# Performance work log

Measured on AMD Instinct MI355X. Metric: run time of the kernel, lower is better.

Reference implementation:

```python
import jax, jax.numpy as jnp
import numpy as np

B, T, C = 16, 2048, 64  # n_embd = 64


def setup_inputs() -> dict:
    key = jax.random.key(0)
    ks = jax.random.split(key, 4)
    scale = 1.0 / np.sqrt(C)
    x = jax.random.normal(ks[0], (B, T, C), dtype=jnp.float32)
    Wk = jax.random.normal(ks[1], (C, C), dtype=jnp.float32) * scale
    Wq = jax.random.normal(ks[2], (C, C), dtype=jnp.float32) * scale
    Wv = jax.random.normal(ks[3], (C, C), dtype=jnp.float32) * scale
    bk = jnp.zeros((C,), dtype=jnp.float32)
    bq = jnp.zeros((C,), dtype=jnp.float32)
    bv = jnp.zeros((C,), dtype=jnp.float32)
    return {"x": x, "Wk": Wk, "bk": bk, "Wq": Wq, "bq": bq, "Wv": Wv, "bv": bv}


def reference(x, Wk, bk, Wq, bq, Wv, bv):
    # Faithful to source: wei = q @ k^T * C**0.5 (MULTIPLY, as in original code),
    # softmax over last axis, no causal mask (tril is built but unused), dropout=0.
    _, _, c = x.shape
    k = jnp.einsum('btc,cd->btd', x, Wk) + bk
    q = jnp.einsum('btc,cd->btd', x, Wq) + bq
    v = jnp.einsum('btc,cd->btd', x, Wv) + bv
    wei = jnp.einsum('btd,bsd->bts', q, k) * (c ** 0.5)  # [B,T,T]
    wei = jax.nn.softmax(wei, axis=-1)
    out = jnp.einsum('bts,bsd->btd', wei, v)  # [B,T,C]
    return out
```

## Files before the change

kernel.cpp:

```cpp
#include <hip/hip_runtime.h>
#include <hip/hip_bf16.h>
#include <stdint.h>

#define NBATCH 16
#define NT 2048
#define NC 64
#define QT 128
#define KT 128
#define SC_LOG2E 11.5415603f

typedef __bf16 bf16x8 __attribute__((ext_vector_type(8)));
typedef float f32x4 __attribute__((ext_vector_type(4)));
typedef float f32x16 __attribute__((ext_vector_type(16)));

#define Z16 {0.f,0.f,0.f,0.f,0.f,0.f,0.f,0.f,0.f,0.f,0.f,0.f,0.f,0.f,0.f,0.f}

extern "C" __device__ float __ocml_native_exp2_f32(float);
#define EXP2F(x) __ocml_native_exp2_f32(x)

static __device__ __forceinline__ unsigned short f2bf(float f) {
  __bf16 h = (__bf16)f;
  union { __bf16 h; unsigned short u; } a; a.h = h; return a.u;
}
static __device__ __forceinline__ float bf2f(unsigned short h) {
  union { uint32_t u; float f; } a; a.u = ((uint32_t)h) << 16;
  return a.f;
}
static __device__ __forceinline__ float fasu(uint32_t u) {
  union { uint32_t u; float f; } a; a.u = u; return a.f;
}
static __device__ __forceinline__ uint32_t uasf(float f) {
  union { float f; uint32_t u; } a; a.f = f; return a.u;
}

#define GLD_LDS16(gsrc, ldst)                                                  \
  __builtin_amdgcn_global_load_lds(                                            \
      (const __attribute__((address_space(1))) void*)(gsrc),                   \
      (__attribute__((address_space(3))) void*)(ldst), 16, 0, 0)

__global__ __launch_bounds__(256, 2) void prep_w(
    const float* __restrict__ Wk, const float* __restrict__ Wq,
    const float* __restrict__ Wv,
    unsigned short* __restrict__ wt_hi, unsigned short* __restrict__ wt_lo)
{
  __shared__ unsigned short hbuf[64][66];
  __shared__ unsigned short lbuf[64][66];
  const int m = (int)blockIdx.x;
  const float* Wm = (m == 0) ? Wk : (m == 1 ? Wq : Wv);
  const int tid = (int)threadIdx.x;
  for (int idx = tid; idx < 1024; idx += 256) {
    int c = idx >> 4, o4 = (idx & 15) * 4;
    float4 v = *(const float4*)(Wm + c * 64 + o4);
    float vals[4] = {v.x, v.y, v.z, v.w};
#pragma unroll
    for (int j = 0; j < 4; ++j) {
      unsigned short h = f2bf(vals[j]);
      hbuf[o4 + j][c] = h;
      lbuf[o4 + j][c] = f2bf(vals[j] - bf2f(h));
    }
  }
  __syncthreads();
  for (int idx = tid; idx < 1024; idx += 256) {
    int o = idx >> 4, c0 = (idx & 15) * 4;
    ushort4 hv, lv;
    hv.x = hbuf[o][c0]; hv.y = hbuf[o][c0 + 1];
    hv.z = hbuf[o][c0 + 2]; hv.w = hbuf[o][c0 + 3];
    lv.x = lbuf[o][c0]; lv.y = lbuf[o][c0 + 1];
    lv.z = lbuf[o][c0 + 2]; lv.w = lbuf[o][c0 + 3];
    *(ushort4*)(wt_hi + (size_t)(m * 64 + o) * 64 + c0) = hv;
    *(ushort4*)(wt_lo + (size_t)(m * 64 + o) * 64 + c0) = lv;
  }
}

__global__ __launch_bounds__(256, 2) void proj_kernel(
    const float* __restrict__ x,
    const unsigned short* __restrict__ wt_hi, const unsigned short* __restrict__ wt_lo,
    const float* __restrict__ bk, const float* __restrict__ bq, const float* __restrict__ bv,
    unsigned short* __restrict__ khi, unsigned short* __restrict__ klo,
    unsigned short* __restrict__ qhi, unsigned short* __restrict__ qlo,
    unsigned short* __restrict__ vt)
{
  __shared__ __align__(16) char smem[65536];
  const int XH = 0, XL = 8192, WTH = 16384, WTL = 40960, VTB = 0;
  const int tid = (int)threadIdx.x;
  const int l = tid & 63, w = tid >> 6;
  const int lr = l & 15, lg = l >> 4;
  const int blk = (int)blockIdx.x;
  const int rowbase = blk * 64;
  const int bb = blk >> 5;

  float4 xv[4];
#pragma unroll
  for (int j = 0; j < 4; ++j) {
    int c = tid + j * 256;
    int row = c >> 4, d0 = (c & 15) * 4;
    xv[j] = *(const float4*)(x + (size_t)(rowbase + row) * NC + d0);
  }
#pragma unroll
  for (int ch4 = 0; ch4 < 6; ++ch4) {
    int ch = ch4 * 4 + w;
    int d = ch * 1024 + l * 16;
    int swk = d ^ (((d >> 7) & 7) << 4);
    GLD_LDS16((const char*)wt_hi + swk, smem + WTH + ch * 1024);
    GLD_LDS16((const char*)wt_lo + swk, smem + WTL + ch * 1024);
  }
#pragma unroll
  for (int j = 0; j < 4; ++j) {
    int c = tid + j * 256;
    int row = c >> 4, d0 = (c & 15) * 4;
    unsigned short h0 = f2bf(xv[j].x), h1 = f2bf(xv[j].y), h2 = f2bf(xv[j].z), h3 = f2bf(xv[j].w);
    unsigned short m0 = f2bf(xv[j].x - bf2f(h0)), m1 = f2bf(xv[j].y - bf2f(h1));
    unsigned short m2 = f2bf(xv[j].z - bf2f(h2)), m3 = f2bf(xv[j].w - bf2f(h3));
    uint2 ph, pl;
    ph.x = (uint32_t)h0 | ((uint32_t)h1 << 16); ph.y = (uint32_t)h2 | ((uint32_t)h3 << 16);
    pl.x = (uint32_t)m0 | ((uint32_t)m1 << 16); pl.y = (uint32_t)m2 | ((uint32_t)m3 << 16);
    int byteoff = (row * 128 + d0 * 2) ^ ((row & 7) << 4);
    *(uint2*)(smem + XH + byteoff) = ph;
    *(uint2*)(smem + XL + byteoff) = pl;
  }
  __syncthreads();

  bf16x8 xh[2], xl[2];
  {
    int row = w * 16 + lr;
#pragma unroll
    for (int dc = 0; dc < 2; ++dc) {
      int byteoff = (row * 128 + (dc * 32 + lg * 8) * 2) ^ ((row & 7) << 4);
      xh[dc] = *(const bf16x8*)(smem + XH + byteoff);
      xl[dc] = *(const bf16x8*)(smem + XL + byteoff);
    }
  }
  f32x4 acc[12];
#pragma unroll
  for (int nb = 0; nb < 12; ++nb) {
    f32x4 a = {0.f, 0.f, 0.f, 0.f};
    int og = nb * 16 + lr;
#pragma unroll
    for (int dc = 0; dc < 2; ++dc) {
      int byteoff = (og * 128 + (dc * 32 + lg * 8) * 2) ^ ((og & 7) << 4);
      bf16x8 bh = *(const bf16x8*)(smem + WTH + byteoff);
      bf16x8 bl = *(const bf16x8*)(smem + WTL + byteoff);
      a = __builtin_amdgcn_mfma_f32_16x16x32_bf16(bh, xh[dc], a, 0, 0, 0);
      a = __builtin_amdgcn_mfma_f32_16x16x32_bf16(bl, xh[dc], a, 0, 0, 0);
      a = __builtin_amdgcn_mfma_f32_16x16x32_bf16(bh, xl[dc], a, 0, 0, 0);
    }
    acc[nb] = a;
  }
  __syncthreads();

  const int tloc = w * 16 + lr;
  const size_t gt = (size_t)(rowbase + tloc);
#pragma unroll
  for (int nb = 0; nb < 12; ++nb) {
    int ogb = (nb & 3) * 16 + lg * 4;
    const float* bp = (nb < 4) ? bk : (nb < 8 ? bq : bv);
    float4 bias = *(const float4*)(bp + ogb);
    float v0 = acc[nb][0] + bias.x, v1 = acc[nb][1] + bias.y,
          v2 = acc[nb][2] + bias.z, v3 = acc[nb][3] + bias.w;
    if (nb < 8) {
      if (nb >= 4) { v0 *= SC_LOG2E; v1 *= SC_LOG2E; v2 *= SC_LOG2E; v3 *= SC_LOG2E; }
      ushort4 hv, lv;
      hv.x = f2bf(v0); lv.x = f2bf(v0 - bf2f(hv.x));
      hv.y = f2bf(v1); lv.y = f2bf(v1 - bf2f(hv.y));
      hv.z = f2bf(v2); lv.z = f2bf(v2 - bf2f(hv.z));
      hv.w = f2bf(v3); lv.w = f2bf(v3 - bf2f(hv.w));
      unsigned short* dH = (nb < 4) ? khi : qhi;
      unsigned short* dL = (nb < 4) ? klo : qlo;
      *(ushort4*)(dH + gt * 64 + ogb) = hv;
      *(ushort4*)(dL + gt * 64 + ogb) = lv;
    } else {
      float vs[4] = {v0, v1, v2, v3};
#pragma unroll
      for (int r = 0; r < 4; ++r) {
        int o = ogb + r;
        int byteoff = (o * 128 + tloc * 2) ^ ((o & 7) << 4);
        *(unsigned short*)(smem + VTB + byteoff) = f2bf(vs[r]);
      }
    }
  }
  __syncthreads();
  for (int cc = tid; cc < 512; cc += 256) {
    int o = cc >> 3, t0 = (cc & 7) * 8;
    int byteoff = (o * 128 + t0 * 2) ^ ((o & 7) << 4);
    uint4 v = *(const uint4*)(smem + VTB + byteoff);
    *(uint4*)(vt + ((size_t)bb * 64 + o) * NT + (size_t)(blk & 31) * 64 + t0) = v;
  }
}

__global__ __launch_bounds__(1024, 4) void attn_kernel(
    const unsigned short* __restrict__ khi, const unsigned short* __restrict__ klo,
    const unsigned short* __restrict__ qhi, const unsigned short* __restrict__ qlo,
    const unsigned short* __restrict__ vt,
    float* __restrict__ out)
{
  __shared__ __align__(16) char smem[98304];
  const int BUF = 49152;
  const int MLB = 65536;
  const int tid = (int)threadIdx.x;
  const int l = tid & 63, w = tid >> 6;
  const int lq = l & 31;
  const bool hi = (l >= 32);
  const int hioff = hi ? 16 : 0;
  const int r = w & 3;
  const int cc = w >> 2;
  const int lb = ((int)(blockIdx.x & 7) << 5) | ((int)blockIdx.x >> 3);
  const int bb = lb >> 4;
  const int qt = lb & 15;

  const char* kh_base = (const char*)(khi + (size_t)bb * NT * 64);
  const char* kl_base = (const char*)(klo + (size_t)bb * NT * 64);
  const char* v_base  = (const char*)(vt + (size_t)bb * 64 * NT);

#define STAGE_TILE(bufp_, it_)                                                 \
  do {                                                                         \
    const char* kh_t = kh_base + (size_t)(it_) * 16384;                        \
    const char* kl_t = kl_base + (size_t)(it_) * 16384;                        \
    const char* v_tb = v_base + (size_t)(it_) * 256;                           \
    int d_ = w * 1024 + l * 16;                                                \
    int swk_ = d_ ^ (((d_ >> 7) & 7) << 4);                                    \
    GLD_LDS16(kh_t + swk_, (bufp_) + w * 1024);                                \
    GLD_LDS16(kl_t + swk_, (bufp_) + 16384 + w * 1024);                        \
    int o_ = d_ >> 8;                                                          \
    int swv_ = (d_ & 255) ^ ((o_ & 7) << 4);                                   \
    GLD_LDS16(v_tb + (size_t)o_ * 4096 + swv_, (bufp_) + 32768 + w * 1024);    \
  } while (0)

  STAGE_TILE(smem, 0);
  bf16x8 Qh[4], Ql[4];
  {
    const char* qh_t = (const char*)qhi + ((size_t)bb * NT + (size_t)qt * QT) * 128;
    const char* ql_t = (const char*)qlo + ((size_t)bb * NT + (size_t)qt * QT) * 128;
    int qrow = r * 32 + lq;
#pragma unroll
    for (int dc = 0; dc < 4; ++dc) {
      Qh[dc] = *(const bf16x8*)(qh_t + qrow * 128 + dc * 32 + hioff);
      Ql[dc] = *(const bf16x8*)(ql_t + qrow * 128 + dc * 32 + hioff);
    }
  }
  asm volatile("s_waitcnt vmcnt(0)" ::: "memory");
  __builtin_amdgcn_s_barrier();
  asm volatile("" ::: "memory");

  f32x16 O0 = Z16, O1 = Z16;
  float mrun = -1e30f, lrun = 0.f;
  const int swr = (lq & 7) << 4;

  for (int it = 0; it < NT / KT; ++it) {
    char* cb = smem + (it & 1) * BUF;
    if (it + 1 < NT / KT) STAGE_TILE(smem + ((it + 1) & 1) * BUF, it + 1);

    f32x16 S = Z16;
    __builtin_amdgcn_s_setprio(1);
#pragma unroll
    for (int dc = 0; dc < 4; ++dc) {
      int krow = cc * 32 + lq;
      int cchunk = (dc * 32 + hioff) ^ swr;
      bf16x8 Ah = *(const bf16x8*)(cb + krow * 128 + cchunk);
      bf16x8 Al = *(const bf16x8*)(cb + 16384 + krow * 128 + cchunk);
      S = __builtin_amdgcn_mfma_f32_32x32x16_bf16(Ah, Qh[dc], S, 0, 0, 0);
      S = __builtin_amdgcn_mfma_f32_32x32x16_bf16(Al, Qh[dc], S, 0, 0, 0);
      S = __builtin_amdgcn_mfma_f32_32x32x16_bf16(Ah, Ql[dc], S, 0, 0, 0);
    }
    __builtin_amdgcn_s_setprio(0);

    float m01 = fmaxf(S[0], S[1]),   m23 = fmaxf(S[2], S[3]);
    float m45 = fmaxf(S[4], S[5]),   m67 = fmaxf(S[6], S[7]);
    float m89 = fmaxf(S[8], S[9]),   mab = fmaxf(S[10], S[11]);
    float mcd = fmaxf(S[12], S[13]), mef = fmaxf(S[14], S[15]);
    float pmax = fmaxf(fmaxf(fmaxf(m01, m23), fmaxf(m45, m67)),
                       fmaxf(fmaxf(m89, mab), fmaxf(mcd, mef)));
    {
      auto sw = __builtin_amdgcn_permlane32_swap(uasf(pmax), uasf(pmax), false, false);
      pmax = fmaxf(fasu(sw[0]), fasu(sw[1]));
    }
    if (__any(pmax > mrun + 11.55f)) {
      float mnew = fmaxf(mrun, pmax);
      float alpha = EXP2F(mrun - mnew);
      O0 *= alpha; O1 *= alpha; lrun *= alpha; mrun = mnew;
    }
    float p[16];
#pragma unroll
    for (int i = 0; i < 16; ++i) p[i] = EXP2F(S[i] - mrun);
    float s01 = p[0] + p[1],   s23 = p[2] + p[3];
    float s45 = p[4] + p[5],   s67 = p[6] + p[7];
    float s89 = p[8] + p[9],   sab = p[10] + p[11];
    float scd = p[12] + p[13], sef = p[14] + p[15];
    float ts = ((s01 + s23) + (s45 + s67)) + ((s89 + sab) + (scd + sef));
    {
      auto sw = __builtin_amdgcn_permlane32_swap(uasf(ts), uasf(ts), false, false);
      ts = fasu(sw[0]) + fasu(sw[1]);
    }
    lrun += ts;

#define PV_CHUNK(kc_)                                                          \
    {                                                                          \
      const int b_ = 8 * (kc_);                                                \
      uint32_t X0, X1, Y0, Y1;                                                 \
      asm("v_cvt_pk_bf16_f32 %0, %1, %2" : "=v"(X0) : "v"(p[b_+0]), "v"(p[b_+1])); \
      asm("v_cvt_pk_bf16_f32 %0, %1, %2" : "=v"(X1) : "v"(p[b_+2]), "v"(p[b_+3])); \
      asm("v_cvt_pk_bf16_f32 %0, %1, %2" : "=v"(Y0) : "v"(p[b_+4]), "v"(p[b_+5])); \
      asm("v_cvt_pk_bf16_f32 %0, %1, %2" : "=v"(Y1) : "v"(p[b_+6]), "v"(p[b_+7])); \
      auto sw0 = __builtin_amdgcn_permlane32_swap(X0, Y0, false, false);       \
      auto sw1 = __builtin_amdgcn_permlane32_swap(X1, Y1, false, false);       \
      union { uint32_t u[4]; bf16x8 v; } cvb;                                  \
      cvb.u[0] = sw0[0]; cvb.u[1] = sw1[0];                                    \
      cvb.u[2] = sw0[1]; cvb.u[3] = sw1[1];                                    \
      bf16x8 Bp = cvb.v;                                                       \
      int vcol = 64 * cc + 32 * (kc_) + hioff;                                 \
      {                                                                        \
        bf16x8 Av = *(const bf16x8*)(cb + 32768 + lq * 256 + (vcol ^ swr));    \
        O0 = __builtin_amdgcn_mfma_f32_32x32x16_bf16(Av, Bp, O0, 0, 0, 0);     \
      }                                                                        \
      {                                                                        \
        bf16x8 Av = *(const bf16x8*)(cb + 32768 + (32 + lq) * 256 + (vcol ^ swr)); \
        O1 = __builtin_amdgcn_mfma_f32_32x32x16_bf16(Av, Bp, O1, 0, 0, 0);     \
      }                                                                        \
    }
    __builtin_amdgcn_s_setprio(1);
    PV_CHUNK(0)
    PV_CHUNK(1)
    __builtin_amdgcn_s_setprio(0);
#undef PV_CHUNK

    asm volatile("s_waitcnt vmcnt(0)" ::: "memory");
    __builtin_amdgcn_s_barrier();
    asm volatile("" ::: "memory");
    __builtin_amdgcn_sched_barrier(0);
  }

  const int lsw = (l & 7) << 4;
#define DUMP(idx_)                                                             \
  {                                                                            \
    char* dd = smem + (idx_) * 8192 + l * 128;                                 \
    _Pragma("unroll")                                                          \
    for (int g = 0; g < 4; ++g) {                                              \
      f32x4 t0, t1;                                                            \
      _Pragma("unroll")                                                        \
      for (int j = 0; j < 4; ++j) { t0[j] = O0[4*g+j]; t1[j] = O1[4*g+j]; }    \
      *(f32x4*)(dd + ((g * 16) ^ lsw)) = t0;                                   \
      *(f32x4*)(dd + ((64 + g * 16) ^ lsw)) = t1;                              \
    }                                                                          \
    *(float*)(smem + MLB + (idx_) * 256 + lq * 8) = mrun;                      \
    *(float*)(smem + MLB + (idx_) * 256 + lq * 8 + 4) = lrun;                  \
  }
#define MERGE(idx_)                                                            \
  {                                                                            \
    const char* ds = smem + (idx_) * 8192 + l * 128;                           \
    float m1 = *(const float*)(smem + MLB + (idx_) * 256 + lq * 8);            \
    float l1 = *(const float*)(smem + MLB + (idx_) * 256 + lq * 8 + 4);        \
    float M = fmaxf(mrun, m1);                                                 \
    float a0 = EXP2F(mrun - M);                                                \
    float a1 = EXP2F(m1 - M);                                                  \
    lrun = lrun * a0 + l1 * a1;                                                \
    mrun = M;                                                                  \
    _Pragma("unroll")                                                          \
    for (int g = 0; g < 4; ++g) {                                              \
      f32x4 o1a = *(const f32x4*)(ds + ((g * 16) ^ lsw));                      \
      f32x4 o1b = *(const f32x4*)(ds + ((64 + g * 16) ^ lsw));                 \
      _Pragma("unroll")                                                        \
      for (int j = 0; j < 4; ++j) {                                            \
        O0[4*g+j] = O0[4*g+j] * a0 + o1a[j] * a1;                              \
        O1[4*g+j] = O1[4*g+j] * a0 + o1b[j] * a1;                              \
      }                                                                        \
    }                                                                          \
  }
  if (cc & 1) DUMP(r * 2 + (cc >> 1));
  __syncthreads();
  if (!(cc & 1)) MERGE(r * 2 + (cc >> 1));
  __syncthreads();
  if (cc == 2) DUMP(r * 2 + 1);
  __syncthreads();
  if (cc == 0) {
    MERGE(r * 2 + 1);
    float inv = 1.0f / lrun;
    float* orow = out + ((size_t)bb * NT + (size_t)qt * QT + r * 32 + lq) * 64;
#pragma unroll
    for (int g = 0; g < 4; ++g) {
      int d0 = 8 * g + (hi ? 4 : 0);
      f32x4 s0, s1;
#pragma unroll
      for (int j = 0; j < 4; ++j) { s0[j] = O0[4*g+j] * inv; s1[j] = O1[4*g+j] * inv; }
      *(f32x4*)(orow + d0) = s0;
      *(f32x4*)(orow + d0 + 32) = s1;
    }
  }
#undef DUMP
#undef MERGE
#undef STAGE_TILE
}

extern "C" void kernel_launch(void* const* d_in, const int* in_sizes, int n_in,
                              void* d_out, int out_size, void* d_ws, size_t ws_size,
                              hipStream_t stream) {
  const float* x  = (const float*)d_in[0];
  const float* Wk = (const float*)d_in[1];
  const float* bk = (const float*)d_in[2];
  const float* Wq = (const float*)d_in[3];
  const float* bq = (const float*)d_in[4];
  const float* Wv = (const float*)d_in[5];
  const float* bv = (const float*)d_in[6];
  float* out = (float*)d_out;

  const size_t NE = (size_t)NBATCH * NT * 64;
  unsigned short* ws = (unsigned short*)d_ws;
  unsigned short* khi = ws;
  unsigned short* klo = ws + NE;
  unsigned short* qhi = ws + 2 * NE;
  unsigned short* qlo = ws + 3 * NE;
  unsigned short* vt  = ws + 4 * NE;
  unsigned short* wt_hi = ws + 5 * NE;
  unsigned short* wt_lo = wt_hi + 192 * 64;

  prep_w<<<dim3(3), dim3(256), 0, stream>>>(Wk, Wq, Wv, wt_hi, wt_lo);
  proj_kernel<<<dim3((NBATCH * NT) / 64), dim3(256), 0, stream>>>(
      x, wt_hi, wt_lo, bk, bq, bv, khi, klo, qhi, qlo, vt);
  attn_kernel<<<dim3(NBATCH * (NT / QT)), dim3(1024), 0, stream>>>(
      khi, klo, qhi, qlo, vt, out);
}
```

Baseline: 67.34 us.

## Switch attention operands to fp16 with single K and two-term Q split

Stores K, Q and V in fp16 rather than bf16. K becomes a single fp16 copy, dropping the K lo term, so QK^T needs two MFMAs per chunk instead of three, and the K staging traffic is halved. The query tile shrinks to 64 rows, with 512-thread blocks and a smaller LDS footprint, giving twice as many blocks. fp16 has less range than bf16, which could matter for the large scaled logits, and the smaller query tile means K/V tiles are reloaded more often per query.

```diff
diff --git a/kernel.cpp b/kernel.cpp
--- a/kernel.cpp
+++ b/kernel.cpp
@@ -5,11 +5,12 @@
 #define NBATCH 16
 #define NT 2048
 #define NC 64
-#define QT 128
+#define QT 64
 #define KT 128
 #define SC_LOG2E 11.5415603f
 
 typedef __bf16 bf16x8 __attribute__((ext_vector_type(8)));
+typedef _Float16 f16x8 __attribute__((ext_vector_type(8)));
 typedef float f32x4 __attribute__((ext_vector_type(4)));
 typedef float f32x16 __attribute__((ext_vector_type(16)));
 
@@ -26,11 +27,22 @@
   union { uint32_t u; float f; } a; a.u = ((uint32_t)h) << 16;
   return a.f;
 }
+static __device__ __forceinline__ unsigned short f2h(float f) {
+  _Float16 h = (_Float16)f;
+  union { _Float16 h; unsigned short u; } a; a.h = h; return a.u;
+}
+static __device__ __forceinline__ float h2f(unsigned short u) {
+  union { unsigned short u; _Float16 h; } a; a.u = u; return (float)a.h;
+}
 static __device__ __forceinline__ float fasu(uint32_t u) {
   union { uint32_t u; float f; } a; a.u = u; return a.f;
 }
 static __device__ __forceinline__ uint32_t uasf(float f) {
   union { float f; uint32_t u; } a; a.f = f; return a.u;
+}
+static __device__ __forceinline__ uint32_t pkh(float a, float b) {
+  auto h = __builtin_amdgcn_cvt_pkrtz(a, b);
+  union { decltype(h) v; uint32_t u; } c; c.v = h; return c.u;
 }
 
 #define GLD_LDS16(gsrc, ldst)                                                  \
@@ -76,9 +88,8 @@
     const float* __restrict__ x,
     const unsigned short* __restrict__ wt_hi, const unsigned short* __restrict__ wt_lo,
     const float* __restrict__ bk, const float* __restrict__ bq, const float* __restrict__ bv,
-    unsigned short* __restrict__ khi, unsigned short* __restrict__ klo,
-    unsigned short* __restrict__ qhi, unsigned short* __restrict__ qlo,
-    unsigned short* __restrict__ vt)
+    unsigned short* __restrict__ kf, unsigned short* __restrict__ qfh,
+    unsigned short* __restrict__ qfl, unsigned short* __restrict__ vt)
 {
   __shared__ __align__(16) char smem[65536];
   const int XH = 0, XL = 8192, WTH = 16384, WTL = 40960, VTB = 0;
@@ -157,24 +168,26 @@
     float4 bias = *(const float4*)(bp + ogb);
     float v0 = acc[nb][0] + bias.x, v1 = acc[nb][1] + bias.y,
           v2 = acc[nb][2] + bias.z, v3 = acc[nb][3] + bias.w;
-    if (nb < 8) {
-      if (nb >= 4) { v0 *= SC_LOG2E; v1 *= SC_LOG2E; v2 *= SC_LOG2E; v3 *= SC_LOG2E; }
+    if (nb < 4) {
+      ushort4 hv;
+      hv.x = f2h(v0); hv.y = f2h(v1); hv.z = f2h(v2); hv.w = f2h(v3);
+      *(ushort4*)(kf + gt * 64 + ogb) = hv;
+    } else if (nb < 8) {
+      v0 *= SC_LOG2E; v1 *= SC_LOG2E; v2 *= SC_LOG2E; v3 *= SC_LOG2E;
       ushort4 hv, lv;
-      hv.x = f2bf(v0); lv.x = f2bf(v0 - bf2f(hv.x));
-      hv.y = f2bf(v1); lv.y = f2bf(v1 - bf2f(hv.y));
-      hv.z = f2bf(v2); lv.z = f2bf(v2 - bf2f(hv.z));
-      hv.w = f2bf(v3); lv.w = f2bf(v3 - bf2f(hv.w));
-      unsigned short* dH = (nb < 4) ? khi : qhi;
-      unsigned short* dL = (nb < 4) ? klo : qlo;
-      *(ushort4*)(dH + gt * 64 + ogb) = hv;
-      *(ushort4*)(dL + gt * 64 + ogb) = lv;
+      hv.x = f2h(v0); lv.x = f2h(v0 - h2f(hv.x));
+      hv.y = f2h(v1); lv.y = f2h(v1 - h2f(hv.y));
+      hv.z = f2h(v2); lv.z = f2h(v2 - h2f(hv.z));
+      hv.w = f2h(v3); lv.w = f2h(v3 - h2f(hv.w));
+      *(ushort4*)(qfh + gt * 64 + ogb) = hv;
+      *(ushort4*)(qfl + gt * 64 + ogb) = lv;
     } else {
       float vs[4] = {v0, v1, v2, v3};
 #pragma unroll
       for (int r = 0; r < 4; ++r) {
         int o = ogb + r;
         int byteoff = (o * 128 + tloc * 2) ^ ((o & 7) << 4);
-        *(unsigned short*)(smem + VTB + byteoff) = f2bf(vs[r]);
+        *(unsigned short*)(smem + VTB + byteoff) = f2h(vs[r]);
       }
     }
   }
@@ -187,54 +200,55 @@
   }
 }
 
-__global__ __launch_bounds__(1024, 4) void attn_kernel(
-    const unsigned short* __restrict__ khi, const unsigned short* __restrict__ klo,
-    const unsigned short* __restrict__ qhi, const unsigned short* __restrict__ qlo,
-    const unsigned short* __restrict__ vt,
+__global__ __launch_bounds__(512, 4) void attn_kernel(
+    const unsigned short* __restrict__ kf, const unsigned short* __restrict__ qfh,
+    const unsigned short* __restrict__ qfl, const unsigned short* __restrict__ vt,
     float* __restrict__ out)
 {
-  __shared__ __align__(16) char smem[98304];
-  const int BUF = 49152;
-  const int MLB = 65536;
+  __shared__ __align__(16) char smem[65536];
+  const int KB_A = 0, KB_B = 16384;
+  const int VB_0 = 32768, VB_1 = 49152;
+  const int MLB = 49152;
   const int tid = (int)threadIdx.x;
   const int l = tid & 63, w = tid >> 6;
   const int lq = l & 31;
   const bool hi = (l >= 32);
   const int hioff = hi ? 16 : 0;
-  const int r = w & 3;
-  const int cc = w >> 2;
-  const int lb = ((int)(blockIdx.x & 7) << 5) | ((int)blockIdx.x >> 3);
-  const int bb = lb >> 4;
-  const int qt = lb & 15;
-
-  const char* kh_base = (const char*)(khi + (size_t)bb * NT * 64);
-  const char* kl_base = (const char*)(klo + (size_t)bb * NT * 64);
-  const char* v_base  = (const char*)(vt + (size_t)bb * 64 * NT);
-
-#define STAGE_TILE(bufp_, it_)                                                 \
+  const int r = w & 1;
+  const int cc = w >> 1;
+  const int lb = ((int)(blockIdx.x & 7) << 6) | ((int)blockIdx.x >> 3);
+  const int bb = lb >> 5;
+  const int qt = lb & 31;
+
+  const char* k_base = (const char*)(kf + (size_t)bb * NT * 64);
+  const char* v_base = (const char*)(vt + (size_t)bb * 64 * NT);
+
+#define STAGE_TILE(kb_, vb_, it_)                                              \
   do {                                                                         \
-    const char* kh_t = kh_base + (size_t)(it_) * 16384;                        \
-    const char* kl_t = kl_base + (size_t)(it_) * 16384;                        \
+    const char* k_t = k_base + (size_t)(it_) * 16384;                          \
     const char* v_tb = v_base + (size_t)(it_) * 256;                           \
-    int d_ = w * 1024 + l * 16;                                                \
-    int swk_ = d_ ^ (((d_ >> 7) & 7) << 4);                                    \
-    GLD_LDS16(kh_t + swk_, (bufp_) + w * 1024);                                \
-    GLD_LDS16(kl_t + swk_, (bufp_) + 16384 + w * 1024);                        \
-    int o_ = d_ >> 8;                                                          \
-    int swv_ = (d_ & 255) ^ ((o_ & 7) << 4);                                   \
-    GLD_LDS16(v_tb + (size_t)o_ * 4096 + swv_, (bufp_) + 32768 + w * 1024);    \
+    _Pragma("unroll")                                                          \
+    for (int j = 0; j < 2; ++j) {                                              \
+      int ch = 2 * w + j;                                                      \
+      int d = ch * 1024 + l * 16;                                              \
+      int swk = d ^ (((d >> 7) & 7) << 4);                                     \
+      GLD_LDS16(k_t + swk, smem + (kb_) + ch * 1024);                          \
+      int o = d >> 8;                                                          \
+      int swv = (d & 255) ^ ((o & 7) << 4);                                    \
+      GLD_LDS16(v_tb + (size_t)o * 4096 + swv, smem + (vb_) + ch * 1024);      \
+    }                                                                          \
   } while (0)
 
-  STAGE_TILE(smem, 0);
-  bf16x8 Qh[4], Ql[4];
+  STAGE_TILE(KB_A, VB_0, 0);
+  f16x8 Qh[4], Ql[4];
   {
-    const char* qh_t = (const char*)qhi + ((size_t)bb * NT + (size_t)qt * QT) * 128;
-    const char* ql_t = (const char*)qlo + ((size_t)bb * NT + (size_t)qt * QT) * 128;
+    const char* qh_t = (const char*)qfh + ((size_t)bb * NT + (size_t)qt * QT) * 128;
+    const char* ql_t = (const char*)qfl + ((size_t)bb * NT + (size_t)qt * QT) * 128;
     int qrow = r * 32 + lq;
 #pragma unroll
     for (int dc = 0; dc < 4; ++dc) {
-      Qh[dc] = *(const bf16x8*)(qh_t + qrow * 128 + dc * 32 + hioff);
-      Ql[dc] = *(const bf16x8*)(ql_t + qrow * 128 + dc * 32 + hioff);
+      Qh[dc] = *(const f16x8*)(qh_t + qrow * 128 + dc * 32 + hioff);
+      Ql[dc] = *(const f16x8*)(ql_t + qrow * 128 + dc * 32 + hioff);
     }
   }
   asm volatile("s_waitcnt vmcnt(0)" ::: "memory");
@@ -246,8 +260,10 @@
   const int swr = (lq & 7) << 4;
 
   for (int it = 0; it < NT / KT; ++it) {
-    char* cb = smem + (it & 1) * BUF;
-    if (it + 1 < NT / KT) STAGE_TILE(smem + ((it + 1) & 1) * BUF, it + 1);
+    const int cbk = (it & 1) ? KB_B : KB_A;
+    const int cbv = (it & 1) ? VB_1 : VB_0;
+    if (it + 1 < NT / KT)
+      STAGE_TILE((it & 1) ? KB_A : KB_B, (it & 1) ? VB_0 : VB_1, it + 1);
 
     f32x16 S = Z16;
     __builtin_amdgcn_s_setprio(1);
@@ -255,20 +271,18 @@
     for (int dc = 0; dc < 4; ++dc) {
       int krow = cc * 32 + lq;
       int cchunk = (dc * 32 + hioff) ^ swr;
-      bf16x8 Ah = *(const bf16x8*)(cb + krow * 128 + cchunk);
-      bf16x8 Al = *(const bf16x8*)(cb + 16384 + krow * 128 + cchunk);
-      S = __builtin_amdgcn_mfma_f32_32x32x16_bf16(Ah, Qh[dc], S, 0, 0, 0);
-      S = __builtin_amdgcn_mfma_f32_32x32x16_bf16(Al, Qh[dc], S, 0, 0, 0);
-      S = __builtin_amdgcn_mfma_f32_32x32x16_bf16(Ah, Ql[dc], S, 0, 0, 0);
+      f16x8 Kf = *(const f16x8*)(smem + cbk + krow * 128 + cchunk);
+      S = __builtin_amdgcn_mfma_f32_32x32x16_f16(Kf, Qh[dc], S, 0, 0, 0);
+      S = __builtin_amdgcn_mfma_f32_32x32x16_f16(Kf, Ql[dc], S, 0, 0, 0);
     }
     __builtin_amdgcn_s_setprio(0);
 
-    float m01 = fmaxf(S[0], S[1]),   m23 = fmaxf(S[2], S[3]);
-    float m45 = fmaxf(S[4], S[5]),   m67 = fmaxf(S[6], S[7]);
-    float m89 = fmaxf(S[8], S[9]),   mab = fmaxf(S[10], S[11]);
-    float mcd = fmaxf(S[12], S[13]), mef = fmaxf(S[14], S[15]);
-    float pmax = fmaxf(fmaxf(fmaxf(m01, m23), fmaxf(m45, m67)),
-                       fmaxf(fmaxf(m89, mab), fmaxf(mcd, mef)));
+    float a01 = fmaxf(S[0], S[1]),   a23 = fmaxf(S[2], S[3]);
+    float a45 = fmaxf(S[4], S[5]),   a67 = fmaxf(S[6], S[7]);
+    float a89 = fmaxf(S[8], S[9]),   aab = fmaxf(S[10], S[11]);
+    float acd = fmaxf(S[12], S[13]), aef = fmaxf(S[14], S[15]);
+    float pmax = fmaxf(fmaxf(fmaxf(a01, a23), fmaxf(a45, a67)),
+                       fmaxf(fmaxf(a89, aab), fmaxf(acd, aef)));
     {
       auto sw = __builtin_amdgcn_permlane32_swap(uasf(pmax), uasf(pmax), false, false);
       pmax = fmaxf(fasu(sw[0]), fasu(sw[1]));
@@ -279,48 +293,35 @@
       O0 *= alpha; O1 *= alpha; lrun *= alpha; mrun = mnew;
     }
     float p[16];
-#pragma unroll
-    for (int i = 0; i < 16; ++i) p[i] = EXP2F(S[i] - mrun);
-    float s01 = p[0] + p[1],   s23 = p[2] + p[3];
-    float s45 = p[4] + p[5],   s67 = p[6] + p[7];
-    float s89 = p[8] + p[9],   sab = p[10] + p[11];
-    float scd = p[12] + p[13], sef = p[14] + p[15];
-    float ts = ((s01 + s23) + (s45 + s67)) + ((s89 + sab) + (scd + sef));
+    float ts = 0.f;
+#pragma unroll
+    for (int i = 0; i < 16; ++i) { p[i] = EXP2F(S[i] - mrun); ts += p[i]; }
     {
       auto sw = __builtin_amdgcn_permlane32_swap(uasf(ts), uasf(ts), false, false);
       ts = fasu(sw[0]) + fasu(sw[1]);
     }
     lrun += ts;
 
-#define PV_CHUNK(kc_)                                                          \
-    {                                                                          \
-      const int b_ = 8 * (kc_);                                                \
-      uint32_t X0, X1, Y0, Y1;                                                 \
-      asm("v_cvt_pk_bf16_f32 %0, %1, %2" : "=v"(X0) : "v"(p[b_+0]), "v"(p[b_+1])); \
-      asm("v_cvt_pk_bf16_f32 %0, %1, %2" : "=v"(X1) : "v"(p[b_+2]), "v"(p[b_+3])); \
-      asm("v_cvt_pk_bf16_f32 %0, %1, %2" : "=v"(Y0) : "v"(p[b_+4]), "v"(p[b_+5])); \
-      asm("v_cvt_pk_bf16_f32 %0, %1, %2" : "=v"(Y1) : "v"(p[b_+6]), "v"(p[b_+7])); \
-      auto sw0 = __builtin_amdgcn_permlane32_swap(X0, Y0, false, false);       \
-      auto sw1 = __builtin_amdgcn_permlane32_swap(X1, Y1, false, false);       \
-      union { uint32_t u[4]; bf16x8 v; } cvb;                                  \
-      cvb.u[0] = sw0[0]; cvb.u[1] = sw1[0];                                    \
-      cvb.u[2] = sw0[1]; cvb.u[3] = sw1[1];                                    \
-      bf16x8 Bp = cvb.v;                                                       \
-      int vcol = 64 * cc + 32 * (kc_) + hioff;                                 \
-      {                                                                        \
-        bf16x8 Av = *(const bf16x8*)(cb + 32768 + lq * 256 + (vcol ^ swr));    \
-        O0 = __builtin_amdgcn_mfma_f32_32x32x16_bf16(Av, Bp, O0, 0, 0, 0);     \
-      }                                                                        \
-      {                                                                        \
-        bf16x8 Av = *(const bf16x8*)(cb + 32768 + (32 + lq) * 256 + (vcol ^ swr)); \
-        O1 = __builtin_amdgcn_mfma_f32_32x32x16_bf16(Av, Bp, O1, 0, 0, 0);     \
-      }                                                                        \
-    }
     __builtin_amdgcn_s_setprio(1);
-    PV_CHUNK(0)
-    PV_CHUNK(1)
+#pragma unroll
+    for (int kc = 0; kc < 2; ++kc) {
+      const int b_ = 8 * kc;
+      uint32_t X0 = pkh(p[b_+0], p[b_+1]);
+      uint32_t X1 = pkh(p[b_+2], p[b_+3]);
+      uint32_t Y0 = pkh(p[b_+4], p[b_+5]);
+      uint32_t Y1 = pkh(p[b_+6], p[b_+7]);
+      auto sw0 = __builtin_amdgcn_permlane32_swap(X0, Y0, false, false);
+      auto sw1 = __builtin_amdgcn_permlane32_swap(X1, Y1, false, false);
+      union { uint32_t u[4]; f16x8 v; } cvb;
+      cvb.u[0] = sw0[0]; cvb.u[1] = sw1[0];
+      cvb.u[2] = sw0[1]; cvb.u[3] = sw1[1];
+      int vcol = 64 * cc + 32 * kc + hioff;
+      f16x8 Av0 = *(const f16x8*)(smem + cbv + lq * 256 + (vcol ^ swr));
+      f16x8 Av1 = *(const f16x8*)(smem + cbv + (32 + lq) * 256 + (vcol ^ swr));
+      O0 = __builtin_amdgcn_mfma_f32_32x32x16_f16(Av0, cvb.v, O0, 0, 0, 0);
+      O1 = __builtin_amdgcn_mfma_f32_32x32x16_f16(Av1, cvb.v, O1, 0, 0, 0);
+    }
     __builtin_amdgcn_s_setprio(0);
-#undef PV_CHUNK
 
     asm volatile("s_waitcnt vmcnt(0)" ::: "memory");
     __builtin_amdgcn_s_barrier();
@@ -403,17 +404,16 @@
 
   const size_t NE = (size_t)NBATCH * NT * 64;
   unsigned short* ws = (unsigned short*)d_ws;
-  unsigned short* khi = ws;
-  unsigned short* klo = ws + NE;
-  unsigned short* qhi = ws + 2 * NE;
-  unsigned short* qlo = ws + 3 * NE;
-  unsigned short* vt  = ws + 4 * NE;
-  unsigned short* wt_hi = ws + 5 * NE;
+  unsigned short* kf  = ws;
+  unsigned short* qfh = ws + NE;
+  unsigned short* qfl = ws + 2 * NE;
+  unsigned short* vt  = ws + 3 * NE;
+  unsigned short* wt_hi = ws + 4 * NE;
   unsigned short* wt_lo = wt_hi + 192 * 64;
 
   prep_w<<<dim3(3), dim3(256), 0, stream>>>(Wk, Wq, Wv, wt_hi, wt_lo);
   proj_kernel<<<dim3((NBATCH * NT) / 64), dim3(256), 0, stream>>>(
-      x, wt_hi, wt_lo, bk, bq, bv, khi, klo, qhi, qlo, vt);
-  attn_kernel<<<dim3(NBATCH * (NT / QT)), dim3(1024), 0, stream>>>(
-      khi, klo, qhi, qlo, vt, out);
-}
+      x, wt_hi, wt_lo, bk, bq, bv, kf, qfh, qfl, vt);
+  attn_kernel<<<dim3(NBATCH * (NT / QT)), dim3(512), 0, stream>>>(
+      kf, qfh, qfl, vt, out);
+}
```

New measurement: 61.54 us. 1.09x faster.
